# Performance work log

Hardware: AMD Instinct MI355X
Metric: run time of the kernel (lower is better)

## Reference

```python
import jax, jax.numpy as jnp
import numpy as np

B, F, SF = 2, 5, 15          # batch, query frames, num_shots*sframe
C, KD, VD = 1024, 128, 512   # encoder_dim, keydim, valdim
H = W = 32                   # l3 feature map (output stride 8 on 256x256)


def _conv(x, w, b, pad):
    y = jax.lax.conv_general_dilated(
        x, w, window_strides=(1, 1), padding=[(pad, pad), (pad, pad)],
        dimension_numbers=("NCHW", "OIHW", "NCHW"))
    return y + b[None, :, None, None]


def setup_inputs() -> dict:
    key = jax.random.key(0)
    ks = jax.random.split(key, 8)
    s = 0.02
    return {
        "query_feat": jax.random.normal(ks[0], (B * F, C, H, W), jnp.float32),
        "support_fg_feat": jax.random.normal(ks[1], (B * SF, C, H, W), jnp.float32),
        "w_sk": jax.random.normal(ks[2], (KD, C, 3, 3), jnp.float32) * s,
        "b_sk": jnp.zeros((KD,), jnp.float32),
        "w_sv": jax.random.normal(ks[3], (VD, C, 3, 3), jnp.float32) * s,
        "b_sv": jnp.zeros((VD,), jnp.float32),
        "w_qq": jax.random.normal(ks[4], (KD, C, 3, 3), jnp.float32) * s,
        "b_qq": jnp.zeros((KD,), jnp.float32),
        "w_qk": jax.random.normal(ks[5], (KD, C, 3, 3), jnp.float32) * s,
        "b_qk": jnp.zeros((KD,), jnp.float32),
        "w_cq": jax.random.normal(ks[6], (VD, C, 1, 1), jnp.float32) * s,
        "b_cq": jnp.zeros((VD,), jnp.float32),
    }


def reference(query_feat, support_fg_feat, w_sk, b_sk, w_sv, b_sv,
              w_qq, b_qq, w_qk, b_qk, w_cq, b_cq):
    hw = H * W
    # QKV projections (3x3 convs)
    sk = _conv(support_fg_feat, w_sk, b_sk, 1)   # [B*SF, KD, H, W]
    sv = _conv(support_fg_feat, w_sv, b_sv, 1)   # [B*SF, VD, H, W]
    qq = _conv(query_feat, w_qq, b_qq, 1)        # [B*F, KD, H, W]
    qk = _conv(query_feat, w_qk, b_qk, 1)        # [B*F, KD, H, W]

    # support K: [B, SF*hw, KD];  support V: [B, VD, SF*hw]
    support_k = sk.reshape(B, SF, KD, H, W).transpose(0, 2, 1, 3, 4)
    support_k = support_k.reshape(B, KD, SF * hw).transpose(0, 2, 1)
    support_v = sv.reshape(B, SF, VD, H, W).transpose(0, 2, 1, 3, 4)
    support_v = support_v.reshape(B, VD, SF * hw)

    qq5 = qq.reshape(B, F, KD, H, W)
    qk5 = qk.reshape(B, F, KD, H, W)
    mid = F // 2
    scale = 1.0 / jnp.sqrt(jnp.float32(KD))

    # stage 1: middle-frame query attends into support memory
    middle_q = qq5[:, mid].reshape(B, KD, hw)                 # [B, KD, hw]
    P1 = jnp.einsum("bkc,bcq->bkq", support_k, middle_q) * scale  # [B, SF*hw, hw]
    P1 = jax.nn.softmax(P1, axis=1)
    new_V = jnp.einsum("bvk,bkq->bvq", support_v, P1)          # [B, VD, hw]

    # stage 2: all-frame queries attend into middle-frame keys
    middle_K = qk5[:, mid].reshape(B, KD, hw).transpose(0, 2, 1)   # [B, hw, KD]
    qq_flat = qq5.transpose(0, 2, 1, 3, 4).reshape(B, KD, F * hw)  # [B, KD, F*hw]
    P2 = jnp.einsum("bkc,bcq->bkq", middle_K, qq_flat) * scale     # [B, hw, F*hw]
    P2 = jax.nn.softmax(P2, axis=1)
    Out = jnp.einsum("bvk,bkq->bvq", new_V, P2)                    # [B, VD, F*hw]

    after = Out.reshape(B, VD, F, H, W).transpose(0, 2, 1, 3, 4)
    after = after.reshape(B * F, VD, H, W)
    qf = _conv(query_feat, w_cq, b_cq, 0)                          # [B*F, VD, H, W]
    return jnp.concatenate([after, qf], axis=1)                    # [B*F, 2*VD, H, W]
```

## Files before the change

### kernel.cpp

```cpp
#include <hip/hip_runtime.h>
#include <cstdint>

typedef unsigned short u16;
typedef __attribute__((ext_vector_type(8))) u16 u16x8;
typedef __attribute__((ext_vector_type(4))) u16 u16x4;
typedef __attribute__((ext_vector_type(8))) _Float16 f16x8;
typedef __attribute__((ext_vector_type(4))) float f32x4;

__device__ __forceinline__ u16 f2h(float f) {
  _Float16 h = (_Float16)f;
  return __builtin_bit_cast(u16, h);
}
__device__ __forceinline__ float h2f(u16 b) {
  _Float16 h = __builtin_bit_cast(_Float16, b);
  return (float)h;
}
__device__ __forceinline__ void gll16(const void* g, void* l) {
  auto gp = reinterpret_cast<const __attribute__((address_space(1))) unsigned int*>(
      reinterpret_cast<uintptr_t>(g));
  auto lp = reinterpret_cast<__attribute__((address_space(3))) unsigned int*>(
      reinterpret_cast<uintptr_t>(l));
  __builtin_amdgcn_global_load_lds(gp, lp, 16, 0, 0);
}

__global__ __launch_bounds__(256) void pad_both(const float* __restrict__ qsrc,
                                                const float* __restrict__ ssrc,
                                                u16* __restrict__ PQ,
                                                u16* __restrict__ PS) {
  const int gi = blockIdx.x >> 5;
  const int y  = blockIdx.x & 31;
  const float* in;
  u16* outp;
  int img;
  if (gi < 10) { in = qsrc; outp = PQ; img = gi; }
  else         { in = ssrc; outp = PS; img = gi - 10; }
  __shared__ float tile[32][33];
  const int tid = threadIdx.x;
  u16* base = outp + (long)img * 34 * 34 * 1024;
  const u16x8 z8 = {0, 0, 0, 0, 0, 0, 0, 0};
  {
    u16* r = base + (long)(y + 1) * 34 * 1024;
    if (tid < 128) *(u16x8*)&r[tid * 8] = z8;
    else *(u16x8*)&r[33 * 1024 + (tid - 128) * 8] = z8;
  }
  if (y == 0) {
    for (int i = tid * 8; i < 34816; i += 2048) *(u16x8*)&base[i] = z8;
  }
  if (y == 31) {
    u16* r = base + 33L * 34 * 1024;
    for (int i = tid * 8; i < 34816; i += 2048) *(u16x8*)&r[i] = z8;
  }
  const int xi = tid & 31, ci = tid >> 5;
  const int xo = tid >> 3, q = tid & 7;
  const float* ip = in + (long)img * 1048576 + y * 32;
  u16* op = base + ((long)(y + 1) * 34 + 1) * 1024;
  for (int c0 = 0; c0 < 1024; c0 += 32) {
#pragma unroll
    for (int k2 = 0; k2 < 4; k2++)
      tile[k2 * 8 + ci][xi] = ip[(long)(c0 + k2 * 8 + ci) * 1024 + xi];
    __syncthreads();
    u16x4 o4;
#pragma unroll
    for (int r = 0; r < 4; r++) o4[r] = f2h(tile[q * 4 + r][xo]);
    *(u16x4*)&op[(long)xo * 1024 + c0 + q * 4] = o4;
    __syncthreads();
  }
}

__device__ __forceinline__ void wre3_body(const float* __restrict__ wp,
                                          u16* __restrict__ op, float* buf) {
  for (int i = threadIdx.x; i < 9216; i += 256) buf[i] = wp[i];
  __syncthreads();
  for (int k = threadIdx.x; k < 9216; k += 256) {
    const int cblk = k / 576;
    const int r = k - cblk * 576;
    const int t = r >> 6, ci = r & 63;
    op[k] = f2h(buf[(cblk * 64 + ci) * 9 + t]);
  }
}
__global__ __launch_bounds__(256) void wprep(
    const float* __restrict__ w_sk, const float* __restrict__ w_sv,
    const float* __restrict__ w_qq, const float* __restrict__ w_qk,
    const float* __restrict__ w_cq, u16* __restrict__ WTSK,
    u16* __restrict__ WTSV, u16* __restrict__ WTQQK, u16* __restrict__ WCQ) {
  __shared__ float buf[9216];
  const int b = blockIdx.x;
  if (b < 128) {
    wre3_body(w_sk + (long)b * 9216, WTSK + (long)b * 9216, buf);
  } else if (b < 640) {
    const int oc = b - 128;
    wre3_body(w_sv + (long)oc * 9216, WTSV + (long)oc * 9216, buf);
  } else if (b < 768) {
    const int oc = b - 640;
    wre3_body(w_qq + (long)oc * 9216, WTQQK + (long)oc * 9216, buf);
  } else if (b < 896) {
    const int oc = b - 768;
    wre3_body(w_qk + (long)oc * 9216, WTQQK + (long)(oc + 128) * 9216, buf);
  } else {
    const int i = (b - 896) * 1024 + threadIdx.x * 4;
#pragma unroll
    for (int r = 0; r < 4; r++) WCQ[i + r] = f2h(w_cq[i + r]);
  }
}

__global__ __launch_bounds__(256) void rowsum60(const u16* __restrict__ P,
                                                float* __restrict__ D) {
  const u16* p = P + (long)blockIdx.x * 15360;
  const int tid = threadIdx.x;
  __shared__ float rs[4];
  float s = 0.f;
  for (int i = tid; i < 1920; i += 256) {
    u16x8 v = *(const u16x8*)(p + (i << 3));
#pragma unroll
    for (int j = 0; j < 8; j++) s += h2f(v[j]);
  }
#pragma unroll
  for (int o = 32; o > 0; o >>= 1) s += __shfl_xor(s, o, 64);
  if ((tid & 63) == 0) rs[tid >> 6] = s;
  __syncthreads();
  if (tid == 0) D[blockIdx.x] = rs[0] + rs[1] + rs[2] + rs[3];
}
__global__ __launch_bounds__(256) void rowsum4(const u16* __restrict__ P,
                                               float* __restrict__ D) {
  const u16* p = P + (long)blockIdx.x * 1024;
  const int tid = threadIdx.x;
  __shared__ float rs[4];
  u16x4 v = *(const u16x4*)(p + (tid << 2));
  float s = h2f(v[0]) + h2f(v[1]) + h2f(v[2]) + h2f(v[3]);
#pragma unroll
  for (int o = 32; o > 0; o >>= 1) s += __shfl_xor(s, o, 64);
  if ((tid & 63) == 0) rs[tid >> 6] = s;
  __syncthreads();
  if (tid == 0) D[blockIdx.x] = rs[0] + rs[1] + rs[2] + rs[3];
}

__global__ __launch_bounds__(256) void reduce8h(const u16* __restrict__ part,
                                                const float* __restrict__ D,
                                                u16* __restrict__ o) {
  long j = ((long)blockIdx.x * 256 + threadIdx.x) * 4;
  int b = (int)(j >> 19);
  long i = j & 524287;
  int q = (int)(i & 1023);
  const u16* p = part + (long)b * 4194304 + i;
  float s0 = 0.f, s1 = 0.f, s2 = 0.f, s3 = 0.f;
#pragma unroll
  for (int c = 0; c < 8; c++) {
    u16x4 v = *(const u16x4*)&p[(long)c * 524288];
    s0 += h2f(v[0]); s1 += h2f(v[1]); s2 += h2f(v[2]); s3 += h2f(v[3]);
  }
  f32x4 dv = *(const f32x4*)&D[b * 1024 + q];
  u16x4 o4 = {f2h(s0 / dv[0]), f2h(s1 / dv[1]), f2h(s2 / dv[2]),
              f2h(s3 / dv[3])};
  *(u16x4*)&o[j] = o4;
}
__global__ __launch_bounds__(256) void reduce_sk(const float* __restrict__ part,
                                                 const float* __restrict__ bias,
                                                 u16* __restrict__ o) {
  long i = ((long)blockIdx.x * 256 + threadIdx.x) * 4;
  f32x4 s = *(const f32x4*)&part[i];
  s = s + *(const f32x4*)&part[i + 3932160];
  f32x4 bb = *(const f32x4*)&bias[(int)(i & 127)];
  u16x4 o4;
#pragma unroll
  for (int r = 0; r < 4; r++) o4[r] = f2h(s[r] + bb[r]);
  *(u16x4*)&o[i] = o4;
}
__global__ __launch_bounds__(256) void reduce_qqk(
    const float* __restrict__ part, const float* __restrict__ b_qq,
    const float* __restrict__ b_qk, u16* __restrict__ QQR,
    u16* __restrict__ QKR) {
  long i = ((long)blockIdx.x * 256 + threadIdx.x) * 4;
  const int n = (int)(i >> 8), m = (int)(i & 255);
  f32x4 s = *(const f32x4*)&part[i];
  s = s + *(const f32x4*)&part[i + 2621440];
  const int lo = (m < 128);
  const int mm = m & 127;
  const float* bs = lo ? b_qq : b_qk;
  f32x4 bb = *(const f32x4*)&bs[mm];
  u16* dst = (lo ? QQR : QKR) + (long)n * 128 + mm;
  u16x4 o4;
#pragma unroll
  for (int r = 0; r < 4; r++) o4[r] = f2h(s[r] + bb[r]);
  *(u16x4*)dst = o4;
}

__global__ __launch_bounds__(512, 1)
void gemm256(const u16* __restrict__ A, const u16* __restrict__ B,
             const float* __restrict__ bias, u16* __restrict__ out) {
  __shared__ u16 lds[81920];
  const int tid = threadIdx.x, lane = tid & 63, wave = tid >> 6;
  const int nwg = gridDim.x * gridDim.y;
  int wg = blockIdx.x + gridDim.x * blockIdx.y;
  wg = (wg & 7) * (nwg >> 3) + (wg >> 3);
  const int ntile = wg % gridDim.x;
  const int mtile = wg / gridDim.x;

  const int slog = (lane & 7) ^ ((lane >> 3) & 7);
  const u16* aS[4];
  const u16* bS[4];
  int aD[4], bD[4];
#pragma unroll
  for (int j = 0; j < 4; j++) {
    const int r = wave * 32 + j * 8 + (lane >> 3);
    aS[j] = A + (long)(mtile * 256 + r) * 9216 + slog * 8;
    aD[j] = (wave * 32 + j * 8) * 64;
    const int n = ntile * 256 + r;
    const int img = n >> 10, p = n & 1023;
    const int y = p >> 5, x = p & 31;
    bS[j] = B + ((long)((img * 34 + y) * 34 + x)) * 1024 + slog * 8;
    bD[j] = (wave * 32 + j * 8) * 64;
  }

  const int g = lane >> 4, l15 = lane & 15;
  const int wm = wave >> 2, wn = wave & 3;
  int aRow[8], bRow[4], sx[2];
#pragma unroll
  for (int mi = 0; mi < 8; mi++) aRow[mi] = (wm * 128 + mi * 16 + l15) * 64;
#pragma unroll
  for (int ni = 0; ni < 4; ni++) bRow[ni] = (wn * 64 + ni * 16 + l15) * 64;
#pragma unroll
  for (int ks = 0; ks < 2; ks++) sx[ks] = ((ks * 4 + g) ^ (l15 & 7)) * 8;

  auto conv_badd = [](int kt) {
    const int cblk = kt / 9;
    const int t = kt - cblk * 9;
    const int dy = t / 3, dx = t - dy * 3;
    return (dy * 34 + dx) * 1024 + cblk * 64;
  };

  f32x4 acc[8][4];
  const f32x4 zero = {0.f, 0.f, 0.f, 0.f};
#pragma unroll
  for (int i = 0; i < 8; i++)
#pragma unroll
    for (int j = 0; j < 4; j++) acc[i][j] = zero;

  const int nkt = 144;
  {
#pragma unroll
    for (int j = 0; j < 4; j++) gll16(aS[j], &lds[aD[j]]);
    const int b0o = conv_badd(0), b1o = conv_badd(1);
#pragma unroll
    for (int j = 0; j < 4; j++) gll16(bS[j] + b0o, &lds[32768 + bD[j]]);
#pragma unroll
    for (int j = 0; j < 4; j++) gll16(bS[j] + b1o, &lds[49152 + bD[j]]);
    asm volatile("s_waitcnt vmcnt(4)" ::: "memory");
    __builtin_amdgcn_s_barrier();
  }

  f16x8 a0[4], a1[4], a3[4], b0[4], b2[4];
  f16x8 zf;
#pragma unroll
  for (int j = 0; j < 8; j++) zf[j] = (_Float16)0.0f;
#pragma unroll
  for (int i = 0; i < 4; i++) { a3[i] = zf; b2[i] = zf; }

  int bc = 0;
  for (int kt = 0; kt < nkt; ++kt) {
    const int abuf = (kt & 1) << 14;
    const int anbuf = abuf ^ 16384;
    const int bbuf = 32768 + bc * 16384;
    int bsn = bc + 2; if (bsn >= 3) bsn -= 3;
    const int bnbuf = 32768 + bsn * 16384;
    const bool stA = (kt + 1 < nkt);
    const bool stB = (kt + 2 < nkt);
    const int kA = (kt + 1) << 6;
    const int bAdd2 = stB ? conv_badd(kt + 2) : 0;

#pragma unroll
    for (int i = 0; i < 4; i++) a0[i] = *(const f16x8*)&lds[abuf + aRow[i] + sx[0]];
#pragma unroll
    for (int i = 0; i < 4; i++) b0[i] = *(const f16x8*)&lds[bbuf + bRow[i] + sx[0]];
#pragma unroll
    for (int i = 0; i < 4; i++) a1[i] = *(const f16x8*)&lds[abuf + aRow[i + 4] + sx[0]];
#pragma unroll
    for (int mi = 0; mi < 4; mi++)
#pragma unroll
      for (int ni = 0; ni < 4; ni++)
        acc[mi + 4][ni] = __builtin_amdgcn_mfma_f32_16x16x32_f16(
            a3[mi], b2[ni], acc[mi + 4][ni], 0, 0, 0);
    if (stA) {
#pragma unroll
      for (int j = 0; j < 4; j++) gll16(aS[j] + kA, &lds[anbuf + aD[j]]);
    }
#pragma unroll
    for (int mi = 0; mi < 4; mi++)
#pragma unroll
      for (int ni = 0; ni < 4; ni++)
        acc[mi][ni] = __builtin_amdgcn_mfma_f32_16x16x32_f16(
            a0[mi], b0[ni], acc[mi][ni], 0, 0, 0);
#pragma unroll
    for (int i = 0; i < 4; i++) a0[i] = *(const f16x8*)&lds[abuf + aRow[i] + sx[1]];
#pragma unroll
    for (int i = 0; i < 4; i++) b2[i] = *(const f16x8*)&lds[bbuf + bRow[i] + sx[1]];
    if (stB) {
#pragma unroll
      for (int j = 0; j < 4; j++) gll16(bS[j] + bAdd2, &lds[bnbuf + bD[j]]);
    }
#pragma unroll
    for (int mi = 0; mi < 4; mi++)
#pragma unroll
      for (int ni = 0; ni < 4; ni++)
        acc[mi + 4][ni] = __builtin_amdgcn_mfma_f32_16x16x32_f16(
            a1[mi], b0[ni], acc[mi + 4][ni], 0, 0, 0);
#pragma unroll
    for (int i = 0; i < 4; i++) a3[i] = *(const f16x8*)&lds[abuf + aRow[i + 4] + sx[1]];
#pragma unroll
    for (int mi = 0; mi < 4; mi++)
#pragma unroll
      for (int ni = 0; ni < 4; ni++)
        acc[mi][ni] = __builtin_amdgcn_mfma_f32_16x16x32_f16(
            a0[mi], b2[ni], acc[mi][ni], 0, 0, 0);
    if (stB) {
      asm volatile("s_waitcnt vmcnt(4)" ::: "memory");
    } else if (stA) {
      asm volatile("s_waitcnt vmcnt(0)" ::: "memory");
    }
    __builtin_amdgcn_s_barrier();
    bc = bc + 1; if (bc >= 3) bc -= 3;
  }
#pragma unroll
  for (int mi = 0; mi < 4; mi++)
#pragma unroll
    for (int ni = 0; ni < 4; ni++)
      acc[mi + 4][ni] = __builtin_amdgcn_mfma_f32_16x16x32_f16(
          a3[mi], b2[ni], acc[mi + 4][ni], 0, 0, 0);

#pragma unroll
  for (int mi = 0; mi < 8; mi++) {
#pragma unroll
    for (int ni = 0; ni < 4; ni++) {
      f32x4 v = acc[mi][ni];
      const int m0 = mtile * 256 + wm * 128 + mi * 16 + g * 4;
      const int n = ntile * 256 + wn * 64 + ni * 16 + l15;
      const int b = (n >= 15360) ? 1 : 0;
      const int rem = n - b * 15360;
#pragma unroll
      for (int r = 0; r < 4; r++) {
        const int m = m0 + r;
        out[(long)b * 7864320 + (long)m * 15360 + rem] = f2h(v[r] + bias[m]);
      }
    }
  }
}

template <int BMODE, int EPI, int SPLITK>
__global__ __launch_bounds__(256, 2)
void gemm_nt(const u16* __restrict__ A, long Azoff, int Astride,
             const u16* __restrict__ B, long Bzoff, int Bstride,
             int K, float scale,
             const float* __restrict__ bias, const float* __restrict__ bias2,
             void* __restrict__ out0, void* __restrict__ out1,
             long out_zoff, int ldo, float cexp = 0.f) {
  __shared__ u16 lds[4 * 8192];
  const int tid = threadIdx.x;
  const int lane = tid & 63;
  const int wave = tid >> 6;
  const int mtile = blockIdx.y, ntile = blockIdx.x, z = blockIdx.z;

  const int zb = (SPLITK > 1) ? z / SPLITK : z;
  const int zc = (SPLITK > 1) ? z % SPLITK : 0;
  const u16* Ab = A + (long)zb * Azoff + (long)zc * K;
  const u16* Bb = B + (long)zb * Bzoff + ((BMODE == 0) ? (long)zc * K : 0);

  const int r8 = lane >> 3;
  const int sphys = lane & 7;
  const u16* aSrc[4];
  const u16* bSrc[4];
  u16* aDst[4];
  u16* bDst[4];
#pragma unroll
  for (int i = 0; i < 4; i++) {
    const int row = wave * 32 + i * 8 + r8;
    const int slog = sphys ^ (row & 7);
    aSrc[i] = Ab + (long)(mtile * 128 + row) * Astride + slog * 8;
    if (BMODE == 0) {
      bSrc[i] = Bb + (long)(ntile * 128 + row) * Bstride + slog * 8;
    } else {
      const int n = ntile * 128 + row;
      const int img = n >> 10;
      const int p = n & 1023;
      const int y = p >> 5, x = p & 31;
      bSrc[i] = Bb + ((long)(img * 34 + y) * 34 + x) * 1024 + slog * 8;
    }
    aDst[i] = &lds[0] + (wave * 32 + i * 8) * 64;
    bDst[i] = &lds[0] + 8192 + (wave * 32 + i * 8) * 64;
  }

  const int g = lane >> 4, l15 = lane & 15;
  const int wm = wave >> 1, wn = wave & 1;
  int offA[2][4], offB[2][4];
#pragma unroll
  for (int ks = 0; ks < 2; ks++) {
    const int sl = ks * 4 + g;
#pragma unroll
    for (int i = 0; i < 4; i++) {
      const int ra = wm * 64 + i * 16 + l15;
      offA[ks][i] = ra * 64 + ((sl ^ (ra & 7)) * 8);
      const int rb = wn * 64 + i * 16 + l15;
      offB[ks][i] = 8192 + rb * 64 + ((sl ^ (rb & 7)) * 8);
    }
  }

  auto stage = [&](int buf, int kb) {
    int bAdd;
    if (BMODE == 0) {
      bAdd = kb;
    } else if (BMODE == 1) {
      const int ktg = (zc * K + kb) >> 6;
      const int cblk = ktg / 9;
      const int t = ktg - cblk * 9;
      const int dy = t / 3, dx = t - dy * 3;
      bAdd = (dy * 34 + dx) * 1024 + cblk * 64;
    } else {
      bAdd = 35 * 1024 + kb;
    }
    const int bufo = buf * 16384;
#pragma unroll
    for (int i = 0; i < 4; i++) gll16(aSrc[i] + kb, aDst[i] + bufo);
#pragma unroll
    for (int i = 0; i < 4; i++) gll16(bSrc[i] + bAdd, bDst[i] + bufo);
  };

  f32x4 acc[4][4];
  const f32x4 zero = {0.f, 0.f, 0.f, 0.f};
#pragma unroll
  for (int i = 0; i < 4; i++)
#pragma unroll
    for (int j = 0; j < 4; j++) acc[i][j] = zero;

  const int nkt = K >> 6;
  stage(0, 0);
  __syncthreads();
  for (int kt = 0; kt < nkt; ++kt) {
    const int buf = kt & 1;
    if (kt + 1 < nkt) stage(buf ^ 1, (kt + 1) << 6);
#pragma unroll
    for (int ks = 0; ks < 2; ks++) {
      f16x8 af[4], bfg[4];
#pragma unroll
      for (int i = 0; i < 4; i++)
        af[i] = *(const f16x8*)&lds[buf * 16384 + offA[ks][i]];
#pragma unroll
      for (int i = 0; i < 4; i++)
        bfg[i] = *(const f16x8*)&lds[buf * 16384 + offB[ks][i]];
#pragma unroll
      for (int mi = 0; mi < 4; mi++)
#pragma unroll
        for (int ni = 0; ni < 4; ni++)
          acc[mi][ni] = __builtin_amdgcn_mfma_f32_16x16x32_f16(
              af[mi], bfg[ni], acc[mi][ni], 0, 0, 0);
    }
    __syncthreads();
  }

#pragma unroll
  for (int mi = 0; mi < 4; mi++) {
#pragma unroll
    for (int ni = 0; ni < 4; ni++) {
      f32x4 v = acc[mi][ni];
      const int m0 = mtile * 128 + wm * 64 + mi * 16 + g * 4;
      const int n = ntile * 128 + wn * 64 + ni * 16 + l15;
      if (EPI == 0) {
        u16* ob = (u16*)out0;
        const float* bs = bias;
        int mm = m0;
        if (out1 != nullptr && m0 >= 128) { ob = (u16*)out1; bs = bias2; mm = m0 - 128; }
        u16x4 pk;
#pragma unroll
        for (int r = 0; r < 4; r++) {
          float val = v[r] * scale + (bs ? bs[mm + r] : 0.f);
          pk[r] = f2h(val);
        }
        *(u16x4*)&ob[(long)n * ldo + mm] = pk;
      } else if (EPI == 1) {
        u16* ob = (u16*)out0 + (long)z * out_zoff;
#pragma unroll
        for (int r = 0; r < 4; r++) {
          const int m = m0 + r;
          float val = v[r] * scale + (bias ? bias[m] : 0.f);
          ob[(long)m * ldo + n] = f2h(val);
        }
      } else if (EPI == 2) {
        float* of = (float*)out0;
        const int img = n >> 10, p = n & 1023;
#pragma unroll
        for (int r = 0; r < 4; r++) {
          const int m = m0 + r;
          of[(long)img * 1048576 + (long)(512 + m) * 1024 + p] =
              v[r] + (bias ? bias[m] : 0.f);
        }
      } else if (EPI == 3) {
        float* of = (float*)out0;
        const int f = n >> 10, p = n & 1023;
        const float dinv = 1.0f / bias2[(long)z * 5120 + n];
#pragma unroll
        for (int r = 0; r < 4; r++) {
          const int m = m0 + r;
          of[(long)z * 5242880 + (long)f * 1048576 + (long)m * 1024 + p] =
              v[r] * dinv;
        }
      } else if (EPI == 4) {
        float* of = (float*)out0 + (long)z * out_zoff;
#pragma unroll
        for (int r = 0; r < 4; r++) of[(long)(m0 + r) * ldo + n] = v[r];
      } else if (EPI == 5) {
        float* of = (float*)out0 + (long)zc * out_zoff;
        *(f32x4*)&of[(long)n * ldo + m0] = v;
      } else if (EPI == 6) {
        u16* ob = (u16*)out0 + (long)z * out_zoff;
#pragma unroll
        for (int r = 0; r < 4; r++) ob[(long)(m0 + r) * ldo + n] = f2h(v[r]);
      } else {
        u16* ob = (u16*)out0 + (long)z * out_zoff;
#pragma unroll
        for (int r = 0; r < 4; r++) {
          const int m = m0 + r;
          ob[(long)m * ldo + n] = f2h(__expf(v[r] * scale - cexp));
        }
      }
    }
  }
}

extern "C" void kernel_launch(void* const* d_in, const int* in_sizes, int n_in,
                              void* d_out, int out_size, void* d_ws, size_t ws_size,
                              hipStream_t stream) {
  (void)in_sizes; (void)n_in; (void)out_size;
  const float* query   = (const float*)d_in[0];
  const float* support = (const float*)d_in[1];
  const float* w_sk = (const float*)d_in[2];  const float* b_sk = (const float*)d_in[3];
  const float* w_sv = (const float*)d_in[4];  const float* b_sv = (const float*)d_in[5];
  const float* w_qq = (const float*)d_in[6];  const float* b_qq = (const float*)d_in[7];
  const float* w_qk = (const float*)d_in[8];  const float* b_qk = (const float*)d_in[9];
  const float* w_cq = (const float*)d_in[10]; const float* b_cq = (const float*)d_in[11];
  float* out = (float*)d_out;
  char* ws = (char*)d_ws;

  if (ws_size < 158924800u) return;

  u16* PQ    = (u16*)(ws + 0);
  u16* PS    = (u16*)(ws + 23674880);
  u16* WTSK  = (u16*)(ws + 94699520);
  u16* WTSV  = (u16*)(ws + 97058816);
  u16* WTQQK = (u16*)(ws + 106496000);
  u16* WCQ   = (u16*)(ws + 111214592);
  u16* SKR   = (u16*)(ws + 112263168);
  u16* SVA   = (u16*)(ws + 120127488);
  u16* QQR   = (u16*)(ws + 151584768);
  u16* QKR   = (u16*)(ws + 154206208);
  u16* NEWV  = (u16*)(ws + 156827648);
  u16* P1T   = PS;
  u16* P2T   = PQ;
  u16* PART2 = (u16*)(ws + 94699520);
  float* PARTK = (float*)SVA;
  float* PARTQ = (float*)SVA;
  float* D1 = (float*)(ws + 112263168);
  float* D2 = D1 + 2048;

  const float SCALE = 0.08838834764831843f;

  pad_both<<<dim3(1280), 256, 0, stream>>>(query, support, PQ, PS);
  wprep<<<dim3(1408), 256, 0, stream>>>(w_sk, w_sv, w_qq, w_qk, w_cq,
                                        WTSK, WTSV, WTQQK, WCQ);

  gemm_nt<1, 5, 2><<<dim3(240, 1, 2), 256, 0, stream>>>(
      WTSK, 0, 9216, PS, 0, 0, 4608, 1.0f, nullptr, nullptr, PARTK, nullptr,
      3932160L, 128);
  reduce_sk<<<dim3(3840), 256, 0, stream>>>(PARTK, b_sk, SKR);

  gemm_nt<1, 5, 2><<<dim3(80, 2, 2), 256, 0, stream>>>(
      WTQQK, 0, 9216, PQ, 0, 0, 4608, 1.0f, nullptr, nullptr, PARTQ, nullptr,
      2621440L, 256);
  reduce_qqk<<<dim3(2560), 256, 0, stream>>>(PARTQ, b_qq, b_qk, QQR, QKR);

  gemm256<<<dim3(120, 2), 512, 0, stream>>>(WTSV, PS, b_sv, SVA);

  gemm_nt<2, 2, 1><<<dim3(80, 4, 1), 256, 0, stream>>>(
      WCQ, 0, 1024, PQ, 0, 0, 1024, 1.0f, b_cq, nullptr, out, nullptr, 0, 0);

  gemm_nt<0, 7, 1><<<dim3(120, 8, 2), 256, 0, stream>>>(
      QQR + 262144, 655360L, 128, SKR, 1966080L, 128, 128, SCALE, nullptr,
      nullptr, P1T, nullptr, 15728640L, 15360, 12.0f);
  rowsum60<<<dim3(2048), 256, 0, stream>>>(P1T, D1);
  gemm_nt<0, 6, 8><<<dim3(8, 4, 16), 256, 0, stream>>>(
      SVA, 7864320L, 15360, P1T, 15728640L, 15360, 1920, 1.0f, nullptr,
      nullptr, PART2, nullptr, 524288L, 1024);
  reduce8h<<<dim3(1024), 256, 0, stream>>>(PART2, D1, NEWV);

  gemm_nt<0, 7, 1><<<dim3(8, 40, 2), 256, 0, stream>>>(
      QQR, 655360L, 128, QKR + 262144, 655360L, 128, 128, SCALE, nullptr,
      nullptr, P2T, nullptr, 5242880L, 1024, 10.0f);
  rowsum4<<<dim3(10240), 256, 0, stream>>>(P2T, D2);
  gemm_nt<0, 3, 1><<<dim3(40, 4, 2), 256, 0, stream>>>(
      NEWV, 524288L, 1024, P2T, 5242880L, 1024, 1024, 1.0f, nullptr, D2,
      out, nullptr, 0, 0);
}
```

Baseline: 593.9 us.

## Load conv B operand directly from global into registers, bypassing LDS

The implicit-GEMM conv kernel stops staging the im2col B tile through a triple-buffered LDS ring. Each lane now loads its MFMA B fragments straight from global memory into registers, prefetching the next tap one iteration ahead with register double-buffering. LDS shrinks to the A double buffer only, which removes B LDS writes and reads. In exchange, B data is no longer shared across the waves that reuse it, so global/L2 traffic rises. The loop also waits on vmcnt(0) every iteration, which may expose global load latency.

```diff
diff --git a/kernel.cpp b/kernel.cpp
--- a/kernel.cpp
+++ b/kernel.cpp
@@ -187,7 +187,7 @@
 __global__ __launch_bounds__(512, 1)
 void gemm256(const u16* __restrict__ A, const u16* __restrict__ B,
              const float* __restrict__ bias, u16* __restrict__ out) {
-  __shared__ u16 lds[81920];
+  __shared__ u16 lds[32768];
   const int tid = threadIdx.x, lane = tid & 63, wave = tid >> 6;
   const int nwg = gridDim.x * gridDim.y;
   int wg = blockIdx.x + gridDim.x * blockIdx.y;
@@ -197,31 +197,32 @@
 
   const int slog = (lane & 7) ^ ((lane >> 3) & 7);
   const u16* aS[4];
-  const u16* bS[4];
-  int aD[4], bD[4];
+  int aD[4];
 #pragma unroll
   for (int j = 0; j < 4; j++) {
     const int r = wave * 32 + j * 8 + (lane >> 3);
     aS[j] = A + (long)(mtile * 256 + r) * 9216 + slog * 8;
     aD[j] = (wave * 32 + j * 8) * 64;
-    const int n = ntile * 256 + r;
+  }
+
+  const int g = lane >> 4, l15 = lane & 15;
+  const int wm = wave >> 2, wn = wave & 3;
+  int aRow[8], sx[2];
+#pragma unroll
+  for (int mi = 0; mi < 8; mi++) aRow[mi] = (wm * 128 + mi * 16 + l15) * 64;
+#pragma unroll
+  for (int ks = 0; ks < 2; ks++) sx[ks] = ((ks * 4 + g) ^ (l15 & 7)) * 8;
+
+  const u16* bped[4];
+#pragma unroll
+  for (int ni = 0; ni < 4; ni++) {
+    const int n = ntile * 256 + wn * 64 + ni * 16 + l15;
     const int img = n >> 10, p = n & 1023;
     const int y = p >> 5, x = p & 31;
-    bS[j] = B + ((long)((img * 34 + y) * 34 + x)) * 1024 + slog * 8;
-    bD[j] = (wave * 32 + j * 8) * 64;
-  }
-
-  const int g = lane >> 4, l15 = lane & 15;
-  const int wm = wave >> 2, wn = wave & 3;
-  int aRow[8], bRow[4], sx[2];
-#pragma unroll
-  for (int mi = 0; mi < 8; mi++) aRow[mi] = (wm * 128 + mi * 16 + l15) * 64;
-#pragma unroll
-  for (int ni = 0; ni < 4; ni++) bRow[ni] = (wn * 64 + ni * 16 + l15) * 64;
-#pragma unroll
-  for (int ks = 0; ks < 2; ks++) sx[ks] = ((ks * 4 + g) ^ (l15 & 7)) * 8;
-
-  auto conv_badd = [](int kt) {
+    bped[ni] = B + ((long)((img * 34 + y) * 34 + x)) * 1024 + g * 8;
+  }
+
+  auto tapoff = [](int kt) {
     const int cblk = kt / 9;
     const int t = kt - cblk * 9;
     const int dy = t / 3, dx = t - dy * 3;
@@ -235,96 +236,91 @@
 #pragma unroll
     for (int j = 0; j < 4; j++) acc[i][j] = zero;
 
-  const int nkt = 144;
+  f16x8 b0X[4], b0Y[4], b1[4], a3[4];
+  f16x8 zf;
+#pragma unroll
+  for (int j = 0; j < 8; j++) zf[j] = (_Float16)0.0f;
+#pragma unroll
+  for (int i = 0; i < 4; i++) { a3[i] = zf; b1[i] = zf; }
+
   {
 #pragma unroll
     for (int j = 0; j < 4; j++) gll16(aS[j], &lds[aD[j]]);
-    const int b0o = conv_badd(0), b1o = conv_badd(1);
-#pragma unroll
-    for (int j = 0; j < 4; j++) gll16(bS[j] + b0o, &lds[32768 + bD[j]]);
-#pragma unroll
-    for (int j = 0; j < 4; j++) gll16(bS[j] + b1o, &lds[49152 + bD[j]]);
-    asm volatile("s_waitcnt vmcnt(4)" ::: "memory");
+    const int t0 = tapoff(0);
+#pragma unroll
+    for (int ni = 0; ni < 4; ni++) b0X[ni] = *(const f16x8*)(bped[ni] + t0);
+    asm volatile("s_waitcnt vmcnt(0)" ::: "memory");
     __builtin_amdgcn_s_barrier();
   }
 
-  f16x8 a0[4], a1[4], a3[4], b0[4], b2[4];
-  f16x8 zf;
-#pragma unroll
-  for (int j = 0; j < 8; j++) zf[j] = (_Float16)0.0f;
-#pragma unroll
-  for (int i = 0; i < 4; i++) { a3[i] = zf; b2[i] = zf; }
-
-  int bc = 0;
-  for (int kt = 0; kt < nkt; ++kt) {
+  auto body = [&](int kt, f16x8 (&bc)[4], f16x8 (&bn)[4]) {
     const int abuf = (kt & 1) << 14;
     const int anbuf = abuf ^ 16384;
-    const int bbuf = 32768 + bc * 16384;
-    int bsn = bc + 2; if (bsn >= 3) bsn -= 3;
-    const int bnbuf = 32768 + bsn * 16384;
-    const bool stA = (kt + 1 < nkt);
-    const bool stB = (kt + 2 < nkt);
-    const int kA = (kt + 1) << 6;
-    const int bAdd2 = stB ? conv_badd(kt + 2) : 0;
-
-#pragma unroll
-    for (int i = 0; i < 4; i++) a0[i] = *(const f16x8*)&lds[abuf + aRow[i] + sx[0]];
-#pragma unroll
-    for (int i = 0; i < 4; i++) b0[i] = *(const f16x8*)&lds[bbuf + bRow[i] + sx[0]];
-#pragma unroll
-    for (int i = 0; i < 4; i++) a1[i] = *(const f16x8*)&lds[abuf + aRow[i + 4] + sx[0]];
+    const bool stA = (kt + 1 < 144);
+    f16x8 a0[4], a1[4];
 #pragma unroll
     for (int mi = 0; mi < 4; mi++)
 #pragma unroll
       for (int ni = 0; ni < 4; ni++)
         acc[mi + 4][ni] = __builtin_amdgcn_mfma_f32_16x16x32_f16(
-            a3[mi], b2[ni], acc[mi + 4][ni], 0, 0, 0);
+            a3[mi], b1[ni], acc[mi + 4][ni], 0, 0, 0);
     if (stA) {
+      const int kA = (kt + 1) << 6;
 #pragma unroll
       for (int j = 0; j < 4; j++) gll16(aS[j] + kA, &lds[anbuf + aD[j]]);
     }
+    {
+      const int to = tapoff(kt);
+#pragma unroll
+      for (int ni = 0; ni < 4; ni++)
+        b1[ni] = *(const f16x8*)(bped[ni] + to + 32);
+      if (stA) {
+        const int tn = tapoff(kt + 1);
+#pragma unroll
+        for (int ni = 0; ni < 4; ni++)
+          bn[ni] = *(const f16x8*)(bped[ni] + tn);
+      }
+    }
+#pragma unroll
+    for (int i = 0; i < 4; i++) a0[i] = *(const f16x8*)&lds[abuf + aRow[i] + sx[0]];
 #pragma unroll
     for (int mi = 0; mi < 4; mi++)
 #pragma unroll
       for (int ni = 0; ni < 4; ni++)
         acc[mi][ni] = __builtin_amdgcn_mfma_f32_16x16x32_f16(
-            a0[mi], b0[ni], acc[mi][ni], 0, 0, 0);
-#pragma unroll
-    for (int i = 0; i < 4; i++) a0[i] = *(const f16x8*)&lds[abuf + aRow[i] + sx[1]];
-#pragma unroll
-    for (int i = 0; i < 4; i++) b2[i] = *(const f16x8*)&lds[bbuf + bRow[i] + sx[1]];
-    if (stB) {
-#pragma unroll
-      for (int j = 0; j < 4; j++) gll16(bS[j] + bAdd2, &lds[bnbuf + bD[j]]);
-    }
+            a0[mi], bc[ni], acc[mi][ni], 0, 0, 0);
+#pragma unroll
+    for (int i = 0; i < 4; i++) a1[i] = *(const f16x8*)&lds[abuf + aRow[i + 4] + sx[0]];
 #pragma unroll
     for (int mi = 0; mi < 4; mi++)
 #pragma unroll
       for (int ni = 0; ni < 4; ni++)
         acc[mi + 4][ni] = __builtin_amdgcn_mfma_f32_16x16x32_f16(
-            a1[mi], b0[ni], acc[mi + 4][ni], 0, 0, 0);
-#pragma unroll
-    for (int i = 0; i < 4; i++) a3[i] = *(const f16x8*)&lds[abuf + aRow[i + 4] + sx[1]];
+            a1[mi], bc[ni], acc[mi + 4][ni], 0, 0, 0);
+#pragma unroll
+    for (int i = 0; i < 4; i++) a0[i] = *(const f16x8*)&lds[abuf + aRow[i] + sx[1]];
 #pragma unroll
     for (int mi = 0; mi < 4; mi++)
 #pragma unroll
       for (int ni = 0; ni < 4; ni++)
         acc[mi][ni] = __builtin_amdgcn_mfma_f32_16x16x32_f16(
-            a0[mi], b2[ni], acc[mi][ni], 0, 0, 0);
-    if (stB) {
-      asm volatile("s_waitcnt vmcnt(4)" ::: "memory");
-    } else if (stA) {
-      asm volatile("s_waitcnt vmcnt(0)" ::: "memory");
-    }
+            a0[mi], b1[ni], acc[mi][ni], 0, 0, 0);
+#pragma unroll
+    for (int i = 0; i < 4; i++) a3[i] = *(const f16x8*)&lds[abuf + aRow[i + 4] + sx[1]];
+    asm volatile("s_waitcnt vmcnt(0)" ::: "memory");
     __builtin_amdgcn_s_barrier();
-    bc = bc + 1; if (bc >= 3) bc -= 3;
+  };
+
+  for (int kt2 = 0; kt2 < 144; kt2 += 2) {
+    body(kt2, b0X, b0Y);
+    body(kt2 + 1, b0Y, b0X);
   }
 #pragma unroll
   for (int mi = 0; mi < 4; mi++)
 #pragma unroll
     for (int ni = 0; ni < 4; ni++)
       acc[mi + 4][ni] = __builtin_amdgcn_mfma_f32_16x16x32_f16(
-          a3[mi], b2[ni], acc[mi + 4][ni], 0, 0, 0);
+          a3[mi], b1[ni], acc[mi + 4][ni], 0, 0, 0);
 
 #pragma unroll
   for (int mi = 0; mi < 8; mi++) {
```

Result: slower. 831.5 us (+40.0%).

## Fuse softmax row sums into exp GEMM epilogue and store split-K partials in fp16

Applied to the files above, without the earlier changes.

The exp-producing GEMM epilogue now accumulates per-row partial sums of the exponentials, reduces them across lanes and waves through LDS, and writes one partial per tile. A small reduceD kernel then combines these partials, replacing the rowsum kernels that re-read the full fp16 probability matrices. Separately, the split-K conv GEMMs write their partial results as fp16 through a new epilogue instead of fp32, halving the partial-buffer traffic. The fp16 partials cost some precision, and the denominators are now summed from fp32 exponentials rather than from the rounded fp16 values stored for the later GEMM.

```diff
diff --git a/kernel.cpp b/kernel.cpp
--- a/kernel.cpp
+++ b/kernel.cpp
@@ -103,35 +103,15 @@
   }
 }
 
-__global__ __launch_bounds__(256) void rowsum60(const u16* __restrict__ P,
-                                                float* __restrict__ D) {
-  const u16* p = P + (long)blockIdx.x * 15360;
-  const int tid = threadIdx.x;
-  __shared__ float rs[4];
-  float s = 0.f;
-  for (int i = tid; i < 1920; i += 256) {
-    u16x8 v = *(const u16x8*)(p + (i << 3));
-#pragma unroll
-    for (int j = 0; j < 8; j++) s += h2f(v[j]);
-  }
+__global__ __launch_bounds__(64) void reduceD(const float* __restrict__ ps,
+                                              float* __restrict__ D, int NT) {
+  const int row = blockIdx.x, tid = threadIdx.x;
+  const float* p = ps + (long)row * NT;
+  float s = (tid < NT) ? p[tid] : 0.f;
+  if (tid + 64 < NT) s += p[tid + 64];
 #pragma unroll
   for (int o = 32; o > 0; o >>= 1) s += __shfl_xor(s, o, 64);
-  if ((tid & 63) == 0) rs[tid >> 6] = s;
-  __syncthreads();
-  if (tid == 0) D[blockIdx.x] = rs[0] + rs[1] + rs[2] + rs[3];
-}
-__global__ __launch_bounds__(256) void rowsum4(const u16* __restrict__ P,
-                                               float* __restrict__ D) {
-  const u16* p = P + (long)blockIdx.x * 1024;
-  const int tid = threadIdx.x;
-  __shared__ float rs[4];
-  u16x4 v = *(const u16x4*)(p + (tid << 2));
-  float s = h2f(v[0]) + h2f(v[1]) + h2f(v[2]) + h2f(v[3]);
-#pragma unroll
-  for (int o = 32; o > 0; o >>= 1) s += __shfl_xor(s, o, 64);
-  if ((tid & 63) == 0) rs[tid >> 6] = s;
-  __syncthreads();
-  if (tid == 0) D[blockIdx.x] = rs[0] + rs[1] + rs[2] + rs[3];
+  if (tid == 0) D[row] = s;
 }
 
 __global__ __launch_bounds__(256) void reduce8h(const u16* __restrict__ part,
@@ -153,26 +133,26 @@
               f2h(s3 / dv[3])};
   *(u16x4*)&o[j] = o4;
 }
-__global__ __launch_bounds__(256) void reduce_sk(const float* __restrict__ part,
+__global__ __launch_bounds__(256) void reduce_sk(const u16* __restrict__ part,
                                                  const float* __restrict__ bias,
                                                  u16* __restrict__ o) {
   long i = ((long)blockIdx.x * 256 + threadIdx.x) * 4;
-  f32x4 s = *(const f32x4*)&part[i];
-  s = s + *(const f32x4*)&part[i + 3932160];
+  u16x4 a = *(const u16x4*)&part[i];
+  u16x4 b = *(const u16x4*)&part[i + 3932160];
   f32x4 bb = *(const f32x4*)&bias[(int)(i & 127)];
   u16x4 o4;
 #pragma unroll
-  for (int r = 0; r < 4; r++) o4[r] = f2h(s[r] + bb[r]);
+  for (int r = 0; r < 4; r++) o4[r] = f2h(h2f(a[r]) + h2f(b[r]) + bb[r]);
   *(u16x4*)&o[i] = o4;
 }
 __global__ __launch_bounds__(256) void reduce_qqk(
-    const float* __restrict__ part, const float* __restrict__ b_qq,
+    const u16* __restrict__ part, const float* __restrict__ b_qq,
     const float* __restrict__ b_qk, u16* __restrict__ QQR,
     u16* __restrict__ QKR) {
   long i = ((long)blockIdx.x * 256 + threadIdx.x) * 4;
   const int n = (int)(i >> 8), m = (int)(i & 255);
-  f32x4 s = *(const f32x4*)&part[i];
-  s = s + *(const f32x4*)&part[i + 2621440];
+  u16x4 a = *(const u16x4*)&part[i];
+  u16x4 b = *(const u16x4*)&part[i + 2621440];
   const int lo = (m < 128);
   const int mm = m & 127;
   const float* bs = lo ? b_qq : b_qk;
@@ -180,7 +160,7 @@
   u16* dst = (lo ? QQR : QKR) + (long)n * 128 + mm;
   u16x4 o4;
 #pragma unroll
-  for (int r = 0; r < 4; r++) o4[r] = f2h(s[r] + bb[r]);
+  for (int r = 0; r < 4; r++) o4[r] = f2h(h2f(a[r]) + h2f(b[r]) + bb[r]);
   *(u16x4*)dst = o4;
 }
 
@@ -454,6 +434,14 @@
     __syncthreads();
   }
 
+  float rp[4][4];
+  if (EPI == 7) {
+#pragma unroll
+    for (int a = 0; a < 4; a++)
+#pragma unroll
+      for (int b = 0; b < 4; b++) rp[a][b] = 0.f;
+  }
+
 #pragma unroll
   for (int mi = 0; mi < 4; mi++) {
 #pragma unroll
@@ -511,14 +499,45 @@
         u16* ob = (u16*)out0 + (long)z * out_zoff;
 #pragma unroll
         for (int r = 0; r < 4; r++) ob[(long)(m0 + r) * ldo + n] = f2h(v[r]);
-      } else {
+      } else if (EPI == 7) {
         u16* ob = (u16*)out0 + (long)z * out_zoff;
 #pragma unroll
         for (int r = 0; r < 4; r++) {
           const int m = m0 + r;
-          ob[(long)m * ldo + n] = f2h(__expf(v[r] * scale - cexp));
+          float e = __expf(v[r] * scale - cexp);
+          ob[(long)m * ldo + n] = f2h(e);
+          rp[mi][r] += e;
         }
+      } else {
+        u16* ob = (u16*)out0 + (long)zc * out_zoff;
+        u16x4 pk;
+#pragma unroll
+        for (int r = 0; r < 4; r++) pk[r] = f2h(v[r]);
+        *(u16x4*)&ob[(long)n * ldo + m0] = pk;
       }
+    }
+  }
+
+  if (EPI == 7) {
+    float* ps = (float*)lds;
+#pragma unroll
+    for (int mi = 0; mi < 4; mi++) {
+#pragma unroll
+      for (int r = 0; r < 4; r++) {
+        float s = rp[mi][r];
+        s += __shfl_xor(s, 1, 64);
+        s += __shfl_xor(s, 2, 64);
+        s += __shfl_xor(s, 4, 64);
+        s += __shfl_xor(s, 8, 64);
+        if (l15 == 0) ps[wn * 128 + wm * 64 + mi * 16 + g * 4 + r] = s;
+      }
+    }
+    __syncthreads();
+    if (tid < 128) {
+      float s = ps[tid] + ps[128 + tid];
+      const int MR = gridDim.y << 7;
+      float* PS = (float*)out1;
+      PS[((long)z * MR + mtile * 128 + tid) * gridDim.x + ntile] = s;
     }
   }
 }
@@ -553,8 +572,10 @@
   u16* P1T   = PS;
   u16* P2T   = PQ;
   u16* PART2 = (u16*)(ws + 94699520);
-  float* PARTK = (float*)SVA;
-  float* PARTQ = (float*)SVA;
+  u16* PARTKH = SVA;
+  u16* PARTQH = SVA;
+  float* PSUM1 = (float*)(ws + 97058816);
+  float* PSUM2 = (float*)(ws + 94699520);
   float* D1 = (float*)(ws + 112263168);
   float* D2 = D1 + 2048;
 
@@ -564,15 +585,15 @@
   wprep<<<dim3(1408), 256, 0, stream>>>(w_sk, w_sv, w_qq, w_qk, w_cq,
                                         WTSK, WTSV, WTQQK, WCQ);
 
-  gemm_nt<1, 5, 2><<<dim3(240, 1, 2), 256, 0, stream>>>(
-      WTSK, 0, 9216, PS, 0, 0, 4608, 1.0f, nullptr, nullptr, PARTK, nullptr,
+  gemm_nt<1, 8, 2><<<dim3(240, 1, 2), 256, 0, stream>>>(
+      WTSK, 0, 9216, PS, 0, 0, 4608, 1.0f, nullptr, nullptr, PARTKH, nullptr,
       3932160L, 128);
-  reduce_sk<<<dim3(3840), 256, 0, stream>>>(PARTK, b_sk, SKR);
-
-  gemm_nt<1, 5, 2><<<dim3(80, 2, 2), 256, 0, stream>>>(
-      WTQQK, 0, 9216, PQ, 0, 0, 4608, 1.0f, nullptr, nullptr, PARTQ, nullptr,
+  reduce_sk<<<dim3(3840), 256, 0, stream>>>(PARTKH, b_sk, SKR);
+
+  gemm_nt<1, 8, 2><<<dim3(80, 2, 2), 256, 0, stream>>>(
+      WTQQK, 0, 9216, PQ, 0, 0, 4608, 1.0f, nullptr, nullptr, PARTQH, nullptr,
       2621440L, 256);
-  reduce_qqk<<<dim3(2560), 256, 0, stream>>>(PARTQ, b_qq, b_qk, QQR, QKR);
+  reduce_qqk<<<dim3(2560), 256, 0, stream>>>(PARTQH, b_qq, b_qk, QQR, QKR);
 
   gemm256<<<dim3(120, 2), 512, 0, stream>>>(WTSV, PS, b_sv, SVA);
 
@@ -581,8 +602,8 @@
 
   gemm_nt<0, 7, 1><<<dim3(120, 8, 2), 256, 0, stream>>>(
       QQR + 262144, 655360L, 128, SKR, 1966080L, 128, 128, SCALE, nullptr,
-      nullptr, P1T, nullptr, 15728640L, 15360, 12.0f);
-  rowsum60<<<dim3(2048), 256, 0, stream>>>(P1T, D1);
+      nullptr, P1T, PSUM1, 15728640L, 15360, 12.0f);
+  reduceD<<<dim3(2048), 64, 0, stream>>>(PSUM1, D1, 120);
   gemm_nt<0, 6, 8><<<dim3(8, 4, 16), 256, 0, stream>>>(
       SVA, 7864320L, 15360, P1T, 15728640L, 15360, 1920, 1.0f, nullptr,
       nullptr, PART2, nullptr, 524288L, 1024);
@@ -590,8 +611,8 @@
 
   gemm_nt<0, 7, 1><<<dim3(8, 40, 2), 256, 0, stream>>>(
       QQR, 655360L, 128, QKR + 262144, 655360L, 128, 128, SCALE, nullptr,
-      nullptr, P2T, nullptr, 5242880L, 1024, 10.0f);
-  rowsum4<<<dim3(10240), 256, 0, stream>>>(P2T, D2);
+      nullptr, P2T, PSUM2, 5242880L, 1024, 10.0f);
+  reduceD<<<dim3(10240), 64, 0, stream>>>(PSUM2, D2, 8);
   gemm_nt<0, 3, 1><<<dim3(40, 4, 2), 256, 0, stream>>>(
       NEWV, 524288L, 1024, P2T, 5242880L, 1024, 1024, 1.0f, nullptr, D2,
       out, nullptr, 0, 0);
```

Measured after the change: 595.5 us. Within noise of the previous version (+0.3%).
